# Optimization experiments

Measured on AMD Instinct MI355X. Metric: run time of the kernel, lower is better.

## Reference

```python
import jax, jax.numpy as jnp
import numpy as np

B, T, E, NH, VOCAB, MULT = 1, 1024, 768, 12, 32000, 32
N = E * MULT // NH  # 2048
LN_EPS = 1e-5


def setup_inputs() -> dict:
    key = jax.random.key(0)
    ks = jax.random.split(key, 6)
    return {
        "idx": jax.random.randint(ks[0], (B, T), 0, VOCAB),
        "embed": jax.random.normal(ks[1], (VOCAB, E), jnp.float32) * 0.02,
        "encoder": jax.random.normal(ks[2], (NH, E, N), jnp.float32) * 0.02,
        "encoder_v": jax.random.normal(ks[3], (NH, E, N), jnp.float32) * 0.02,
        "decoder": jax.random.normal(ks[4], (NH * N, E), jnp.float32) * 0.02,
        "lm_head": jax.random.normal(ks[5], (VOCAB, E), jnp.float32) * 0.02,
        "ln_w": jnp.ones((E,), jnp.float32),
        "ln_b": jnp.zeros((E,), jnp.float32),
        "n_layer": 6,
    }


def reference(idx, embed, encoder, encoder_v, decoder, lm_head, ln_w, ln_b, n_layer):
    nh, e, n = encoder.shape
    t = idx.shape[1]
    dec = decoder.reshape(nh, n, e)  # flatten order (h, n) -> h*N + n

    def ln(x):
        m = jnp.mean(x, axis=-1, keepdims=True)
        v = jnp.mean(jnp.square(x - m), axis=-1, keepdims=True)
        return (x - m) * jax.lax.rsqrt(v + LN_EPS) * ln_w + ln_b

    causal = jnp.tril(jnp.ones((t, t), bool))  # [T, T]
    scale = 1.0 / np.sqrt(n).astype(np.float32)

    x = ln(embed[idx])  # [B, T, E]  (the unsqueezed head dim broadcasts; keep it squeezed)
    for _ in range(n_layer):
        # encoder projection + ReLU: [B,T,E] x [H,E,N] -> [B,H,T,N]
        x_sparse = jax.nn.relu(jnp.einsum("bte,hen->bhtn", x, encoder))
        # hand-rolled causal attention, Q=K=x_sparse, V=x (broadcast over heads)
        scores = jnp.einsum("bhqn,bhkn->bhqk", x_sparse, x_sparse) * scale
        scores = jnp.where(causal, scores, -jnp.inf)
        attn = jax.nn.softmax(scores, axis=-1)
        y = jnp.einsum("bhqk,bke->bhqe", attn, x)  # [B,H,T,E]
        y = ln(y)
        y_sparse = jax.nn.relu(jnp.einsum("bhte,hen->bhtn", y, encoder_v))
        xy = x_sparse * y_sparse  # [B,H,T,N]; dropout p=0 -> identity
        y_mlp = jnp.einsum("bhtn,hne->bte", xy, dec)  # decoder matmul
        x = ln(x + ln(y_mlp))
    logits = jnp.einsum("bte,ve->btv", x, lm_head)
    return logits
```

## Files before the change

### kernel.cpp

```cpp
#include <hip/hip_runtime.h>

typedef unsigned short u16;
typedef short bf16x8 __attribute__((ext_vector_type(8)));
typedef float f32x4 __attribute__((ext_vector_type(4)));
typedef u16 u16x4 __attribute__((ext_vector_type(4)));

#define TT     1024
#define EE     768
#define NHH    12
#define ND     2048
#define VOC    32000
#define HNN    24576
#define NLAYER 6
#define LN_EPS 1e-5f
#define SPLITK 16

__device__ __forceinline__ float b2f(u16 u){
  unsigned int x = ((unsigned int)u) << 16; float f; __builtin_memcpy(&f, &x, 4); return f;
}
__device__ __forceinline__ u16 f2b(float f){
  unsigned int x; __builtin_memcpy(&x, &f, 4);
  x = x + 0x7fffu + ((x >> 16) & 1u);
  return (u16)(x >> 16);
}

__device__ __forceinline__ void gload16(const void* g, void* lds){
  __builtin_amdgcn_global_load_lds(
      (const __attribute__((address_space(1))) unsigned int*)g,
      (__attribute__((address_space(3))) unsigned int*)(unsigned int)(unsigned long long)lds,
      16, 0, 0);
}

__device__ __forceinline__ bf16x8 ldsr(unsigned addr){
  bf16x8 r;
  asm volatile("ds_read_b128 %0, %1" : "=v"(r) : "v"(addr));
  return r;
}

__device__ __forceinline__ void blk_sum2(float& a, float& b){
  #pragma unroll
  for (int o = 32; o > 0; o >>= 1){ a += __shfl_down(a, o); b += __shfl_down(b, o); }
  __shared__ float sa[4], sb[4];
  int lane = threadIdx.x & 63, wid = threadIdx.x >> 6;
  __syncthreads();
  if (lane == 0){ sa[wid] = a; sb[wid] = b; }
  __syncthreads();
  a = (sa[0] + sa[1]) + (sa[2] + sa[3]);
  b = (sb[0] + sb[1]) + (sb[2] + sb[3]);
}
__device__ __forceinline__ float blk_max(float v){
  #pragma unroll
  for (int o = 32; o > 0; o >>= 1) v = fmaxf(v, __shfl_down(v, o));
  __shared__ float sm[4];
  int lane = threadIdx.x & 63, wid = threadIdx.x >> 6;
  __syncthreads();
  if (lane == 0) sm[wid] = v;
  __syncthreads();
  return fmaxf(fmaxf(sm[0], sm[1]), fmaxf(sm[2], sm[3]));
}
__device__ __forceinline__ float blk_sum(float v){
  #pragma unroll
  for (int o = 32; o > 0; o >>= 1) v += __shfl_down(v, o);
  __shared__ float ss[4];
  int lane = threadIdx.x & 63, wid = threadIdx.x >> 6;
  __syncthreads();
  if (lane == 0) ss[wid] = v;
  __syncthreads();
  return (ss[0] + ss[1]) + (ss[2] + ss[3]);
}

__global__ void transpose_f2b(const float* __restrict__ in, long sIn,
                              u16* __restrict__ out, long sOut, int R, int Cc){
  __shared__ float tile[32][33];
  int z = blockIdx.z;
  in  += (long)z * sIn;
  out += (long)z * sOut;
  int c0 = blockIdx.x * 32, r0 = blockIdx.y * 32;
  int lx = threadIdx.x & 31, ly = threadIdx.x >> 5;
  #pragma unroll
  for (int i = 0; i < 32; i += 8)
    tile[ly + i][lx] = in[(long)(r0 + ly + i) * Cc + (c0 + lx)];
  __syncthreads();
  #pragma unroll
  for (int i = 0; i < 32; i += 8)
    out[(long)(c0 + ly + i) * R + (r0 + lx)] = f2b(tile[lx][ly + i]);
}

__global__ void conv_f2b(const float* __restrict__ in, u16* __restrict__ out){
  long i = ((long)blockIdx.x * 256 + threadIdx.x) * 4;
  float4 v = *(const float4*)(in + i);
  u16x4 o; o.x = f2b(v.x); o.y = f2b(v.y); o.z = f2b(v.z); o.w = f2b(v.w);
  *(u16x4*)(out + i) = o;
}

__global__ void embed_ln(const int* __restrict__ idx, const float* __restrict__ emb,
                         const float* __restrict__ w, const float* __restrict__ b,
                         float* __restrict__ xf, u16* __restrict__ xb, u16* __restrict__ xT){
  int t = blockIdx.x, tid = threadIdx.x;
  const float* src = emb + (long)idx[t] * EE;
  float v[3];
  #pragma unroll
  for (int j = 0; j < 3; j++) v[j] = src[tid + j * 256];
  float s = v[0] + v[1] + v[2];
  float s2 = v[0]*v[0] + v[1]*v[1] + v[2]*v[2];
  blk_sum2(s, s2);
  float m  = s * (1.0f / EE);
  float var = s2 * (1.0f / EE) - m * m;
  float rs = rsqrtf(var + LN_EPS);
  #pragma unroll
  for (int j = 0; j < 3; j++){
    int e = tid + j * 256;
    float o = (v[j] - m) * rs * w[e] + b[e];
    xf[(long)t * EE + e] = o;
    u16 ob = f2b(o);
    xb[(long)t * EE + e] = ob;
    xT[(long)e * TT + t] = ob;
  }
}

__global__ void ln_rows(const float* __restrict__ in, u16* __restrict__ out,
                        const float* __restrict__ w, const float* __restrict__ b){
  long row = blockIdx.x; int tid = threadIdx.x;
  const float* src = in + row * EE;
  float v[3];
  #pragma unroll
  for (int j = 0; j < 3; j++) v[j] = src[tid + j * 256];
  float s = v[0] + v[1] + v[2];
  float s2 = v[0]*v[0] + v[1]*v[1] + v[2]*v[2];
  blk_sum2(s, s2);
  float m = s * (1.0f / EE);
  float var = s2 * (1.0f / EE) - m * m;
  float rs = rsqrtf(var + LN_EPS);
  #pragma unroll
  for (int j = 0; j < 3; j++){
    int e = tid + j * 256;
    out[row * EE + e] = f2b((v[j] - m) * rs * w[e] + b[e]);
  }
}

__global__ void softmax_rows(const float* __restrict__ scores, u16* __restrict__ attn){
  int q = blockIdx.x, h = blockIdx.y, tid = threadIdx.x;
  const float* srow = scores + ((long)h * TT + q) * TT;
  u16* arow = attn + ((long)h * TT + q) * TT;
  float4 v = *(const float4*)(srow + tid * 4);
  float mx = blk_max(fmaxf(fmaxf(v.x, v.y), fmaxf(v.z, v.w)));
  float e0 = __expf(v.x - mx), e1 = __expf(v.y - mx);
  float e2 = __expf(v.z - mx), e3 = __expf(v.w - mx);
  float inv = 1.0f / blk_sum(e0 + e1 + e2 + e3);
  u16x4 o; o.x = f2b(e0 * inv); o.y = f2b(e1 * inv); o.z = f2b(e2 * inv); o.w = f2b(e3 * inv);
  *(u16x4*)(arow + tid * 4) = o;
}

template<int P>
__global__ void residual_ln(const float* __restrict__ part, const float* __restrict__ xin,
                            float* __restrict__ xf, u16* __restrict__ xb, u16* __restrict__ xT,
                            const float* __restrict__ w, const float* __restrict__ b){
  int t = blockIdx.x, tid = threadIdx.x;
  float g[3];
  #pragma unroll
  for (int j = 0; j < 3; j++){
    int e = tid + j * 256;
    float s = 0.f;
    #pragma unroll
    for (int pp = 0; pp < P; pp++) s += part[((long)pp * TT + t) * EE + e];
    g[j] = s;
  }
  float s = g[0] + g[1] + g[2], s2 = g[0]*g[0] + g[1]*g[1] + g[2]*g[2];
  blk_sum2(s, s2);
  float m = s * (1.0f / EE), var = s2 * (1.0f / EE) - m * m;
  float rs = rsqrtf(var + LN_EPS);
  float hh[3];
  #pragma unroll
  for (int j = 0; j < 3; j++){
    int e = tid + j * 256;
    hh[j] = xin[(long)t * EE + e] + ((g[j] - m) * rs * w[e] + b[e]);
  }
  s = hh[0] + hh[1] + hh[2]; s2 = hh[0]*hh[0] + hh[1]*hh[1] + hh[2]*hh[2];
  blk_sum2(s, s2);
  m = s * (1.0f / EE); var = s2 * (1.0f / EE) - m * m; rs = rsqrtf(var + LN_EPS);
  #pragma unroll
  for (int j = 0; j < 3; j++){
    int e = tid + j * 256;
    float o = (hh[j] - m) * rs * w[e] + b[e];
    xf[(long)t * EE + e] = o;
    u16 ob = f2b(o);
    xb[(long)t * EE + e] = ob;
    xT[(long)e * TT + t] = ob;
  }
}

template<int EPI, bool CCLAMP>
__global__ __launch_bounds__(256, 2)
void gemmw(const u16* __restrict__ Ab, long sA,
           const u16* __restrict__ Bb, long sB,
           void* __restrict__ Cb, long sC,
           int grid_m, int grid_mn,
           int K, int lda, int ldb, int ldc, float scale,
           const u16* __restrict__ Mul, long sMul, int ldmul){
  constexpr unsigned BUFB = 24576u;
  __shared__ __align__(16) u16 S[3 * 12288];

  const int nwg = gridDim.x, orig = blockIdx.x;
  const int q = nwg >> 3, r = nwg & 7, xcd = orig & 7;
  const int wgid = (xcd < r ? xcd*(q+1) : r*(q+1) + (xcd - r)*q) + (orig >> 3);
  const int z   = wgid / grid_mn;
  const int rem = wgid - z*grid_mn;
  const int nb  = rem / grid_m;
  const int mb  = rem - nb*grid_m;
  const int m0 = mb*128, n0 = nb*256;
  const int tid = threadIdx.x, lane = tid & 63, wid = tid >> 6;

  if (EPI == 2 && n0 > m0 + 127){
    float* C = (float*)Cb + (long)z * sC;
    #pragma unroll
    for (int i = 0; i < 32; i++){
      int idx4 = (tid + i*256)*4;
      int rr = idx4 >> 8, cc = idx4 & 255;
      *(float4*)&C[(long)(m0+rr)*ldc + n0 + cc] = make_float4(-1e30f,-1e30f,-1e30f,-1e30f);
    }
    return;
  }

  const u16* A = Ab + (long)z*sA;
  const u16* B = Bb + (long)z*sB;

  const int rS = tid >> 2;
  const int cS = (((tid & 3) ^ ((rS >> 1) & 3)) << 3);
  const u16* gA[2]; const u16* gB[4];
  #pragma unroll
  for (int i = 0; i < 2; i++) gA[i] = A + (long)(m0 + i*64 + rS)*lda + cS;
  #pragma unroll
  for (int i = 0; i < 4; i++) gB[i] = B + (long)(n0 + i*64 + rS)*ldb + cS;

  char* Sb = (char*)&S[0];
  auto stage = [&](int kt, unsigned bB){
    const int ko = kt << 5;
    gload16(gA[0] + ko, Sb + bB +          wid*1024u);
    gload16(gA[1] + ko, Sb + bB +  4096u + wid*1024u);
    #pragma unroll
    for (int i = 0; i < 4; i++)
      gload16(gB[i] + ko, Sb + bB + 8192u + i*4096u + wid*1024u);
  };

  const int wr = wid >> 1, wc = wid & 1;
  const int fr = lane & 15, fk = lane >> 4;
  const unsigned base = (unsigned)(unsigned long long)Sb;
  unsigned aAd[4], bAd[8];
  #pragma unroll
  for (int mi = 0; mi < 4; mi++){
    int row = wr*64 + mi*16 + fr;
    aAd[mi] = base + (unsigned)(row*64 + ((fk ^ ((row >> 1) & 3)) << 4));
  }
  #pragma unroll
  for (int ni = 0; ni < 8; ni++){
    int row = wc*128 + ni*16 + fr;
    bAd[ni] = base + 8192u + (unsigned)(row*64 + ((fk ^ ((row >> 1) & 3)) << 4));
  }

  const int Keff = CCLAMP ? (m0 + 128 < K ? m0 + 128 : K) : K;
  const int NT = Keff >> 5;
  const int s0 = (mb*13 + nb*7 + z*5) % NT;

  f32x4 acc[4][8] = {};

  int p1 = s0 + 1; if (p1 >= NT) p1 -= NT;
  stage(s0, 0);
  stage(p1, BUFB);
  asm volatile("s_waitcnt vmcnt(6)" ::: "memory");
  __builtin_amdgcn_s_barrier();
  __builtin_amdgcn_sched_barrier(0);

  unsigned rbB = 0, wbB = 2u*BUFB;
  for (int t = 0; t < NT; t++){
    int nx = (t + 2 < NT) ? t + 2 : NT - 1;
    int ph = s0 + nx; if (ph >= NT) ph -= NT;
    stage(ph, wbB);
    bf16x8 afr[4], bfr[8];
    #pragma unroll
    for (int ni = 0; ni < 8; ni++) bfr[ni] = ldsr(bAd[ni] + rbB);
    #pragma unroll
    for (int mi = 0; mi < 4; mi++) afr[mi] = ldsr(aAd[mi] + rbB);
    __builtin_amdgcn_s_barrier();
    asm volatile("s_waitcnt lgkmcnt(0)" ::: "memory");
    __builtin_amdgcn_sched_barrier(0);
    __builtin_amdgcn_s_setprio(1);
    #pragma unroll
    for (int mi = 0; mi < 4; mi++)
      #pragma unroll
      for (int ni = 0; ni < 8; ni++)
        acc[mi][ni] = __builtin_amdgcn_mfma_f32_16x16x32_bf16(afr[mi], bfr[ni], acc[mi][ni], 0, 0, 0);
    __builtin_amdgcn_s_setprio(0);
    __builtin_amdgcn_sched_barrier(0);
    asm volatile("s_waitcnt vmcnt(6)" ::: "memory");
    __builtin_amdgcn_s_barrier();
    __builtin_amdgcn_sched_barrier(0);
    unsigned tmp = rbB; rbB += BUFB; if (rbB == 3u*BUFB) rbB = 0;
    wbB = tmp;
  }
  asm volatile("s_waitcnt vmcnt(0)" ::: "memory");

  const int er = (lane >> 4) * 4, ec = lane & 15;
  #pragma unroll
  for (int mi = 0; mi < 4; mi++){
    #pragma unroll
    for (int ni = 0; ni < 8; ni++){
      #pragma unroll
      for (int j = 0; j < 4; j++){
        int row = m0 + wr*64 + mi*16 + er + j;
        int col = n0 + wc*128 + ni*16 + ec;
        float v = acc[mi][ni][j];
        if (EPI == 0){
          ((float*)Cb + (long)z * sC)[(long)row * ldc + col] = v;
        } else if (EPI == 1){
          v = v > 0.f ? v : 0.f;
          ((u16*)Cb + (long)z * sC)[(long)row * ldc + col] = f2b(v);
        } else if (EPI == 2){
          v *= scale;
          if (col > row) v = -1e30f;
          ((float*)Cb + (long)z * sC)[(long)row * ldc + col] = v;
        } else {
          v = v > 0.f ? v : 0.f;
          float mfv = b2f((Mul + (long)z * sMul)[(long)row * ldmul + col]);
          ((u16*)Cb + (long)z * sC)[(long)row * ldc + col] = f2b(v * mfv);
        }
      }
    }
  }
}

extern "C" void kernel_launch(void* const* d_in, const int* in_sizes, int n_in,
                              void* d_out, int out_size, void* d_ws, size_t ws_size,
                              hipStream_t stream){
  (void)in_sizes; (void)n_in; (void)out_size; (void)ws_size;
  const int*   idx     = (const int*)  d_in[0];
  const float* embed   = (const float*)d_in[1];
  const float* encoder = (const float*)d_in[2];
  const float* encv    = (const float*)d_in[3];
  const float* decoder = (const float*)d_in[4];
  const float* lm_head = (const float*)d_in[5];
  const float* ln_w    = (const float*)d_in[6];
  const float* ln_b    = (const float*)d_in[7];
  float* out = (float*)d_out;

  char* p = (char*)d_ws;
  auto take = [&](size_t n){ char* r = p; p += (n + 255) & ~(size_t)255; return r; };
  u16*   encT  = (u16*)  take((size_t)NHH * ND * EE * 2);
  u16*   encvT = (u16*)  take((size_t)NHH * ND * EE * 2);
  u16*   decT  = (u16*)  take((size_t)EE * HNN * 2);
  u16*   lmhB  = (u16*)  take((size_t)VOC * EE * 2);
  float* xf    = (float*)take((size_t)TT * EE * 4);
  u16*   xb    = (u16*)  take((size_t)TT * EE * 2);
  u16*   xT    = (u16*)  take((size_t)EE * TT * 2);
  u16*   xs    = (u16*)  take((size_t)NHH * TT * ND * 2);
  char*  big   =         take((size_t)NHH * TT * TT * 4);
  u16*   attn  = (u16*)  take((size_t)NHH * TT * TT * 2);
  u16*   yb    = (u16*)  take((size_t)NHH * TT * EE * 2);
  take((size_t)8 * TT * EE * 4);
  float* scores = (float*)big;
  float* yf     = (float*)big;
  u16*   xy     = (u16*)big;
  float* part   = (float*)attn;

  dim3 blk(256, 1, 1);

  transpose_f2b<<<dim3(ND / 32, EE / 32, NHH), blk, 0, stream>>>(encoder, (long)EE * ND, encT,  (long)ND * EE, EE, ND);
  transpose_f2b<<<dim3(ND / 32, EE / 32, NHH), blk, 0, stream>>>(encv,    (long)EE * ND, encvT, (long)ND * EE, EE, ND);
  transpose_f2b<<<dim3(EE / 32, HNN / 32, 1),  blk, 0, stream>>>(decoder, 0, decT, 0, HNN, EE);
  conv_f2b<<<dim3((VOC * EE) / 1024, 1, 1), blk, 0, stream>>>(lm_head, lmhB);

  embed_ln<<<dim3(TT, 1, 1), blk, 0, stream>>>(idx, embed, ln_w, ln_b, xf, xb, xT);

  const float scl = 0.022097086912079608f;

  for (int L = 0; L < NLAYER; ++L){
    gemmw<1,false><<<dim3(8*8*NHH), blk, 0, stream>>>(
        xb, 0, encT, (long)ND * EE, xs, (long)TT * ND,
        8, 64, EE, EE, EE, ND, 0.f, (const u16*)0, 0, 0);
    gemmw<2,false><<<dim3(8*4*NHH), blk, 0, stream>>>(
        xs, (long)TT * ND, xs, (long)TT * ND, scores, (long)TT * TT,
        8, 32, ND, ND, ND, TT, scl, (const u16*)0, 0, 0);
    softmax_rows<<<dim3(TT, NHH, 1), blk, 0, stream>>>(scores, attn);
    gemmw<0,true><<<dim3(8*3*NHH), blk, 0, stream>>>(
        attn, (long)TT * TT, xT, 0, yf, (long)TT * EE,
        8, 24, TT, TT, TT, EE, 0.f, (const u16*)0, 0, 0);
    ln_rows<<<dim3(NHH * TT, 1, 1), blk, 0, stream>>>(yf, yb, ln_w, ln_b);
    gemmw<3,false><<<dim3(8*8*NHH), blk, 0, stream>>>(
        yb, (long)TT * EE, encvT, (long)ND * EE, xy, (long)ND,
        8, 64, EE, EE, EE, HNN, 0.f, xs, (long)TT * ND, ND);
    gemmw<0,false><<<dim3(8*3*SPLITK), blk, 0, stream>>>(
        xy, (long)(HNN / SPLITK), decT, (long)(HNN / SPLITK), part, (long)TT * EE,
        8, 24, HNN / SPLITK, HNN, HNN, EE, 0.f, (const u16*)0, 0, 0);
    residual_ln<SPLITK><<<dim3(TT, 1, 1), blk, 0, stream>>>(part, xf, xf, xb, xT, ln_w, ln_b);
  }

  gemmw<0,false><<<dim3(8*125), blk, 0, stream>>>(
      xb, 0, lmhB, 0, out, 0,
      8, 1000, EE, EE, EE, VOC, 0.f, (const u16*)0, 0, 0);
}
```

Baseline: 2.033 ms.

## Add 256x256-tile 8-wave GEMM kernel with ping-pong LDS pipeline

Adds a new GEMM kernel with 512 threads and 256x256 output tiles. It double-buffers 64-wide K slices in LDS with interleaved global prefetch, barriers and MFMA priority bumps. The encoder, score, encoder_v and lm_head GEMMs switch to it, which raises data reuse per tile and cuts global traffic. The cost is fewer workgroups (e.g. 384 for the encoder GEMM, 192 for the scores GEMM on 256 CUs), a large LDS footprint and heavy register pressure. The epilogue stores scalars rather than vectors.

```diff
diff --git a/kernel.cpp b/kernel.cpp
--- a/kernel.cpp
+++ b/kernel.cpp
@@ -186,6 +186,194 @@
     u16 ob = f2b(o);
     xb[(long)t * EE + e] = ob;
     xT[(long)e * TT + t] = ob;
+  }
+}
+
+template<int EPI>
+__global__ __launch_bounds__(512, 2)
+void g8(const u16* __restrict__ Ab, long sA,
+        const u16* __restrict__ Bb, long sB,
+        void* __restrict__ Cb, long sC,
+        int grid_m, int grid_mn,
+        int K, int lda, int ldb, int ldc, float scale,
+        const u16* __restrict__ Mul, long sMul, int ldmul){
+  __shared__ __align__(16) u16 S[69632];
+
+  const int nwg = gridDim.x, orig = blockIdx.x;
+  const int q = nwg >> 3, r = nwg & 7, xcd = orig & 7;
+  const int wgid = (xcd < r ? xcd*(q+1) : r*(q+1) + (xcd - r)*q) + (orig >> 3);
+  const int z   = wgid / grid_mn;
+  const int rem = wgid - z*grid_mn;
+  const int nb  = rem / grid_m;
+  const int mb  = rem - nb*grid_m;
+  const int m0 = mb*256, n0 = nb*256;
+  const int tid = threadIdx.x, lane = tid & 63, wid = tid >> 6;
+
+  if (EPI == 2 && n0 > m0 + 255){
+    float* C = (float*)Cb + (long)z * sC;
+    #pragma unroll
+    for (int i = 0; i < 32; i++){
+      int idx4 = (tid + i*512)*4;
+      int rr = idx4 >> 8, cc = idx4 & 255;
+      *(float4*)&C[(long)(m0+rr)*ldc + n0 + cc] = make_float4(-1e30f,-1e30f,-1e30f,-1e30f);
+    }
+    return;
+  }
+
+  const u16* A = Ab + (long)z*sA;
+  const u16* B = Bb + (long)z*sB;
+
+  const int rS = wid*16 + (lane >> 2);
+  const int cS = (((lane & 3) ^ ((rS >> 1) & 3)) << 3);
+  const u16* gA = A + (long)(m0 + rS)*lda + cS;
+  const u16* gB = B + (long)(n0 + rS)*ldb + cS;
+
+  char* Sb = (char*)&S[0];
+  const unsigned db0 = 0, db1 = 65536u, scr = 131072u;
+  auto issue = [&](const u16* src, unsigned dstOff){
+    gload16(src, Sb + dstOff + (unsigned)wid*1024u);
+  };
+
+  const int wr = wid >> 2, wc = wid & 3;
+  const int fr = lane & 15, fk = lane >> 4;
+  const unsigned base = (unsigned)(unsigned long long)Sb;
+  unsigned aOff[8], bOff[4];
+  #pragma unroll
+  for (int mi = 0; mi < 8; mi++){
+    int row = wr*128 + mi*16 + fr;
+    aOff[mi] = (unsigned)(row*64 + ((fk ^ ((row >> 1) & 3)) << 4));
+  }
+  #pragma unroll
+  for (int ni = 0; ni < 4; ni++){
+    int row = wc*64 + ni*16 + fr;
+    bOff[ni] = 32768u + (unsigned)(row*64 + ((fk ^ ((row >> 1) & 3)) << 4));
+  }
+
+  const int NT = K >> 6;
+  const long lda128 = (long)128*lda, ldb128 = (long)128*ldb;
+
+  f32x4 acc[8][4] = {};
+
+  issue(gA,              db0);          issue(gA + lda128,          db0 + 8192u);
+  issue(gB,              db0+32768u);   issue(gB + ldb128,          db0 + 40960u);
+  issue(gA + 32,         db0+16384u);   issue(gA + 32 + lda128,     db0 + 24576u);
+  issue(gB + 32,         db0+49152u);   issue(gB + 32 + ldb128,     db0 + 57344u);
+  issue(gA + 64,         db1);          issue(gA + 64 + lda128,     db1 + 8192u);
+  issue(gB + 64,         db1+32768u);   issue(gB + 64 + ldb128,     db1 + 40960u);
+  asm volatile("s_waitcnt vmcnt(8)" ::: "memory");
+  __builtin_amdgcn_s_barrier();
+  __builtin_amdgcn_sched_barrier(0);
+
+  for (int t = 0; t < NT; t++){
+    const unsigned cur = (t & 1) ? db1 : db0;
+    const unsigned oth = (t & 1) ? db0 : db1;
+    const bool v1 = (t + 1 < NT), v2 = (t + 2 < NT);
+    const long k1 = (long)(v1 ? t + 1 : 0) * 64;
+    const long k2 = (long)(v2 ? t + 2 : 0) * 64;
+    const unsigned d1A = v1 ? oth + 16384u : scr;
+    const unsigned d1B = v1 ? oth + 49152u : scr;
+    const unsigned d2A = v2 ? cur           : scr;
+    const unsigned d2B = v2 ? cur + 32768u  : scr;
+    bf16x8 a[4], b[4];
+
+    #pragma unroll
+    for (int ni = 0; ni < 4; ni++) b[ni] = ldsr(base + cur + bOff[ni]);
+    #pragma unroll
+    for (int u = 0; u < 4; u++)    a[u]  = ldsr(base + cur + aOff[u]);
+    issue(gA + k1 + 32, d1A); issue(gA + k1 + 32 + lda128, d1A + 8192u);
+    __builtin_amdgcn_s_barrier();
+    asm volatile("s_waitcnt lgkmcnt(0)" ::: "memory");
+    __builtin_amdgcn_sched_barrier(0);
+    __builtin_amdgcn_s_setprio(1);
+    #pragma unroll
+    for (int u = 0; u < 4; u++)
+      #pragma unroll
+      for (int ni = 0; ni < 4; ni++)
+        acc[u][ni] = __builtin_amdgcn_mfma_f32_16x16x32_bf16(a[u], b[ni], acc[u][ni], 0, 0, 0);
+    __builtin_amdgcn_s_setprio(0);
+    __builtin_amdgcn_s_barrier();
+    __builtin_amdgcn_sched_barrier(0);
+
+    #pragma unroll
+    for (int u = 0; u < 4; u++) a[u] = ldsr(base + cur + aOff[4 + u]);
+    issue(gB + k1 + 32, d1B); issue(gB + k1 + 32 + ldb128, d1B + 8192u);
+    __builtin_amdgcn_s_barrier();
+    asm volatile("s_waitcnt lgkmcnt(0)" ::: "memory");
+    __builtin_amdgcn_sched_barrier(0);
+    __builtin_amdgcn_s_setprio(1);
+    #pragma unroll
+    for (int u = 0; u < 4; u++)
+      #pragma unroll
+      for (int ni = 0; ni < 4; ni++)
+        acc[4+u][ni] = __builtin_amdgcn_mfma_f32_16x16x32_bf16(a[u], b[ni], acc[4+u][ni], 0, 0, 0);
+    __builtin_amdgcn_s_setprio(0);
+    asm volatile("s_waitcnt vmcnt(8)" ::: "memory");
+    __builtin_amdgcn_s_barrier();
+    __builtin_amdgcn_sched_barrier(0);
+
+    #pragma unroll
+    for (int ni = 0; ni < 4; ni++) b[ni] = ldsr(base + cur + bOff[ni] + 16384u);
+    #pragma unroll
+    for (int u = 0; u < 4; u++)    a[u]  = ldsr(base + cur + aOff[u] + 16384u);
+    issue(gA + k2, d2A); issue(gA + k2 + lda128, d2A + 8192u);
+    __builtin_amdgcn_s_barrier();
+    asm volatile("s_waitcnt lgkmcnt(0)" ::: "memory");
+    __builtin_amdgcn_sched_barrier(0);
+    __builtin_amdgcn_s_setprio(1);
+    #pragma unroll
+    for (int u = 0; u < 4; u++)
+      #pragma unroll
+      for (int ni = 0; ni < 4; ni++)
+        acc[u][ni] = __builtin_amdgcn_mfma_f32_16x16x32_bf16(a[u], b[ni], acc[u][ni], 0, 0, 0);
+    __builtin_amdgcn_s_setprio(0);
+    __builtin_amdgcn_s_barrier();
+    __builtin_amdgcn_sched_barrier(0);
+
+    #pragma unroll
+    for (int u = 0; u < 4; u++) a[u] = ldsr(base + cur + aOff[4 + u] + 16384u);
+    issue(gB + k2, d2B); issue(gB + k2 + ldb128, d2B + 8192u);
+    __builtin_amdgcn_s_barrier();
+    asm volatile("s_waitcnt lgkmcnt(0)" ::: "memory");
+    __builtin_amdgcn_sched_barrier(0);
+    __builtin_amdgcn_s_setprio(1);
+    #pragma unroll
+    for (int u = 0; u < 4; u++)
+      #pragma unroll
+      for (int ni = 0; ni < 4; ni++)
+        acc[4+u][ni] = __builtin_amdgcn_mfma_f32_16x16x32_bf16(a[u], b[ni], acc[4+u][ni], 0, 0, 0);
+    __builtin_amdgcn_s_setprio(0);
+    asm volatile("s_waitcnt vmcnt(8)" ::: "memory");
+    __builtin_amdgcn_s_barrier();
+    __builtin_amdgcn_sched_barrier(0);
+  }
+  asm volatile("s_waitcnt vmcnt(0)" ::: "memory");
+
+  const int er = (lane >> 4) * 4, ec = lane & 15;
+  #pragma unroll
+  for (int mi = 0; mi < 8; mi++){
+    #pragma unroll
+    for (int ni = 0; ni < 4; ni++){
+      #pragma unroll
+      for (int j = 0; j < 4; j++){
+        int row = m0 + wr*128 + mi*16 + er + j;
+        int col = n0 + wc*64 + ni*16 + ec;
+        float v = acc[mi][ni][j];
+        if (EPI == 0){
+          ((float*)Cb + (long)z * sC)[(long)row * ldc + col] = v;
+        } else if (EPI == 1){
+          v = v > 0.f ? v : 0.f;
+          ((u16*)Cb + (long)z * sC)[(long)row * ldc + col] = f2b(v);
+        } else if (EPI == 2){
+          v *= scale;
+          if (col > row) v = -1e30f;
+          ((float*)Cb + (long)z * sC)[(long)row * ldc + col] = v;
+        } else {
+          v = v > 0.f ? v : 0.f;
+          float mfv = b2f((Mul + (long)z * sMul)[(long)row * ldmul + col]);
+          ((u16*)Cb + (long)z * sC)[(long)row * ldc + col] = f2b(v * mfv);
+        }
+      }
+    }
   }
 }
 
@@ -373,27 +561,27 @@
   const float scl = 0.022097086912079608f;
 
   for (int L = 0; L < NLAYER; ++L){
-    gemmw<1,false><<<dim3(8*8*NHH), blk, 0, stream>>>(
+    g8<1><<<dim3(4*8*NHH), dim3(512), 0, stream>>>(
         xb, 0, encT, (long)ND * EE, xs, (long)TT * ND,
-        8, 64, EE, EE, EE, ND, 0.f, (const u16*)0, 0, 0);
-    gemmw<2,false><<<dim3(8*4*NHH), blk, 0, stream>>>(
+        4, 32, EE, EE, EE, ND, 0.f, (const u16*)0, 0, 0);
+    g8<2><<<dim3(4*4*NHH), dim3(512), 0, stream>>>(
         xs, (long)TT * ND, xs, (long)TT * ND, scores, (long)TT * TT,
-        8, 32, ND, ND, ND, TT, scl, (const u16*)0, 0, 0);
+        4, 16, ND, ND, ND, TT, scl, (const u16*)0, 0, 0);
     softmax_rows<<<dim3(TT, NHH, 1), blk, 0, stream>>>(scores, attn);
     gemmw<0,true><<<dim3(8*3*NHH), blk, 0, stream>>>(
         attn, (long)TT * TT, xT, 0, yf, (long)TT * EE,
         8, 24, TT, TT, TT, EE, 0.f, (const u16*)0, 0, 0);
     ln_rows<<<dim3(NHH * TT, 1, 1), blk, 0, stream>>>(yf, yb, ln_w, ln_b);
-    gemmw<3,false><<<dim3(8*8*NHH), blk, 0, stream>>>(
+    g8<3><<<dim3(4*8*NHH), dim3(512), 0, stream>>>(
         yb, (long)TT * EE, encvT, (long)ND * EE, xy, (long)ND,
-        8, 64, EE, EE, EE, HNN, 0.f, xs, (long)TT * ND, ND);
+        4, 32, EE, EE, EE, HNN, 0.f, xs, (long)TT * ND, ND);
     gemmw<0,false><<<dim3(8*3*SPLITK), blk, 0, stream>>>(
         xy, (long)(HNN / SPLITK), decT, (long)(HNN / SPLITK), part, (long)TT * EE,
         8, 24, HNN / SPLITK, HNN, HNN, EE, 0.f, (const u16*)0, 0, 0);
     residual_ln<SPLITK><<<dim3(TT, 1, 1), blk, 0, stream>>>(part, xf, xf, xb, xT, ln_w, ln_b);
   }
 
-  gemmw<0,false><<<dim3(8*125), blk, 0, stream>>>(
+  g8<0><<<dim3(4*125), dim3(512), 0, stream>>>(
       xb, 0, lmhB, 0, out, 0,
-      8, 1000, EE, EE, EE, VOC, 0.f, (const u16*)0, 0, 0);
-}
+      4, 500, EE, EE, EE, VOC, 0.f, (const u16*)0, 0, 0);
+}
```

Measured after the change: 1.992 ms. -2.0%, faster.
